# Kernel optimization log

Measured on AMD Instinct MI355X. Metric: run time of the kernel, lower is better.

## Reference

```python
import jax, jax.numpy as jnp
import numpy as np

D_MODEL = 1024
NUM_HEADS = 16
HEAD_DIM = D_MODEL // NUM_HEADS


def setup_inputs() -> dict:
    key = jax.random.key(0)
    ks = jax.random.split(key, 5)
    B, S = 2, 2048
    x = jax.random.normal(ks[0], (B, S, D_MODEL), dtype=jnp.float32)
    Wq = jax.random.normal(ks[1], (D_MODEL, D_MODEL), dtype=jnp.float32) * 0.02
    Wk = jax.random.normal(ks[2], (D_MODEL, D_MODEL), dtype=jnp.float32) * 0.02
    Wv = jax.random.normal(ks[3], (D_MODEL, D_MODEL), dtype=jnp.float32) * 0.02
    Wo = jax.random.normal(ks[4], (D_MODEL, D_MODEL), dtype=jnp.float32) * 0.02
    return {"x": x, "Wq": Wq, "Wk": Wk, "Wv": Wv, "Wo": Wo}


def reference(x, Wq, Wk, Wv, Wo):
    B, S, _ = x.shape
    # QKV projections (Linear is x @ W, no bias)
    q = (x @ Wq).reshape(B, S, NUM_HEADS, HEAD_DIM).transpose(0, 2, 1, 3)  # [B,H,S,Dh]
    k = (x @ Wk).reshape(B, S, NUM_HEADS, HEAD_DIM).transpose(0, 2, 1, 3)
    v = (x @ Wv).reshape(B, S, NUM_HEADS, HEAD_DIM).transpose(0, 2, 1, 3)
    scale = 1.0 / jnp.sqrt(jnp.asarray(HEAD_DIM, dtype=x.dtype))
    scores = jnp.einsum("bhqd,bhkd->bhqk", q, k) * scale  # [B,H,S,S]
    causal = jnp.tril(jnp.ones((S, S), dtype=bool))
    scores = jnp.where(causal, scores, -jnp.inf)
    probs = jax.nn.softmax(scores, axis=-1)
    out = jnp.einsum("bhqk,bhkd->bhqd", probs, v)  # [B,H,S,Dh]
    out = out.transpose(0, 2, 1, 3).reshape(B, S, D_MODEL)
    return out @ Wo
```

## Files before the change

### kernel.cpp

```cpp
#include <hip/hip_runtime.h>

typedef __attribute__((ext_vector_type(4))) short short4v;
typedef __attribute__((ext_vector_type(8))) short short8v;
typedef __attribute__((ext_vector_type(4))) float float4v;
typedef __attribute__((ext_vector_type(4))) int int4v;

#define GLD_LDS16(gsrc, ldst)                                                             \
    __builtin_amdgcn_global_load_lds(                                                     \
        (const __attribute__((address_space(1))) void*)(gsrc),                            \
        (__attribute__((address_space(3))) void*)(ldst), 16, 0, 0)

__device__ __forceinline__ short f2bf(float f) {
    unsigned u = __builtin_bit_cast(unsigned, f);
    u += 0x7fffu + ((u >> 16) & 1u);
    return (short)(u >> 16);
}

__global__ void k_cvt_x(const float* __restrict__ x, short* __restrict__ xb) {
    int i = blockIdx.x * blockDim.x + threadIdx.x;
    float4v v = ((const float4v*)x)[i];
    short4v o;
    o[0] = f2bf(v[0]); o[1] = f2bf(v[1]); o[2] = f2bf(v[2]); o[3] = f2bf(v[3]);
    ((short4v*)xb)[i] = o;
}

__global__ void k_transpose(const float* __restrict__ W0, const float* __restrict__ W1,
                            const float* __restrict__ W2, const float* __restrict__ W3,
                            short* __restrict__ Wt) {
    const float* W = blockIdx.z == 0 ? W0 : blockIdx.z == 1 ? W1 : blockIdx.z == 2 ? W2 : W3;
    short* dst = Wt + (size_t)blockIdx.z * 1024 * 1024;
    __shared__ float tile[32][33];
    int x0 = blockIdx.x * 32, y0 = blockIdx.y * 32;
    int tx = threadIdx.x, ty = threadIdx.y;
#pragma unroll
    for (int j = 0; j < 4; j++) {
        int r = ty + j * 8;
        tile[r][tx] = W[(size_t)(y0 + r) * 1024 + x0 + tx];
    }
    __syncthreads();
#pragma unroll
    for (int j = 0; j < 4; j++) {
        int r = ty + j * 8;
        dst[(size_t)(x0 + r) * 1024 + y0 + tx] = f2bf(tile[tx][r]);
    }
}

template <int MODE>
__launch_bounds__(512, 4)
__global__ void k_gemm2(const short* __restrict__ A, const short* __restrict__ Bt,
                        short* __restrict__ out0, short* __restrict__ out1,
                        float* __restrict__ outF) {
    __shared__ short As[2][128][64];
    __shared__ short Bs[2][128][64];
    int t = threadIdx.x;
    int l = t & 63, w = t >> 6;
    int wm = w >> 2, wn = w & 3;
    int lr = l & 15, lg = l >> 4;
    int m0 = blockIdx.x * 128, n0 = blockIdx.y * 128;
    const short* Bp = Bt + (MODE == 0 ? ((size_t)blockIdx.z << 20) : 0);

    int srow = l >> 3;
    int sg = (l & 7) ^ srow;
    const short* Ab0 = A + (size_t)(m0 + w * 8 + srow) * 1024 + sg * 8;
    const short* Ab1 = Ab0 + 64 * 1024;
    const short* Bb0 = Bp + (size_t)(n0 + w * 8 + srow) * 1024 + sg * 8;
    const short* Bb1 = Bb0 + 64 * 1024;

    float4v acc[4][2] = {};

#define STAGE(bb, k0)                                   \
    do {                                                \
        GLD_LDS16(Ab0 + (k0), &As[bb][w * 8][0]);       \
        GLD_LDS16(Ab1 + (k0), &As[bb][64 + w * 8][0]);  \
        GLD_LDS16(Bb0 + (k0), &Bs[bb][w * 8][0]);       \
        GLD_LDS16(Bb1 + (k0), &Bs[bb][64 + w * 8][0]);  \
    } while (0)

    STAGE(0, 0);
    __syncthreads();
    int cur = 0;

    for (int kt = 0; kt < 16; kt++) {
        if (kt + 1 < 16) STAGE(cur ^ 1, (kt + 1) * 64);
#pragma unroll
        for (int ks = 0; ks < 2; ks++) {
            short8v af[4], bfv[2];
            int hh = ks * 4 + lg;
            int sw = ((hh ^ (lr & 7)) * 8);
#pragma unroll
            for (int fm = 0; fm < 4; fm++)
                af[fm] = *(const short8v*)&As[cur][wm * 64 + fm * 16 + lr][sw];
#pragma unroll
            for (int fn = 0; fn < 2; fn++)
                bfv[fn] = *(const short8v*)&Bs[cur][wn * 32 + fn * 16 + lr][sw];
            __builtin_amdgcn_s_setprio(1);
#pragma unroll
            for (int fm = 0; fm < 4; fm++)
#pragma unroll
                for (int fn = 0; fn < 2; fn++)
                    acc[fm][fn] = (MODE == 1)
                        ? __builtin_amdgcn_mfma_f32_16x16x32_bf16(bfv[fn], af[fm], acc[fm][fn], 0, 0, 0)
                        : __builtin_amdgcn_mfma_f32_16x16x32_bf16(af[fm], bfv[fn], acc[fm][fn], 0, 0, 0);
            __builtin_amdgcn_s_setprio(0);
        }
        __syncthreads();
        cur ^= 1;
    }
#undef STAGE

    if (MODE == 0) {
        short* out = (blockIdx.z == 0) ? out0 : out1;
        float scale = (blockIdx.z == 0) ? 0.125f * 1.44269504088896f : 1.0f;
#pragma unroll
        for (int fm = 0; fm < 4; fm++)
#pragma unroll
            for (int fn = 0; fn < 2; fn++)
#pragma unroll
                for (int r = 0; r < 4; r++) {
                    int m = m0 + wm * 64 + fm * 16 + lg * 4 + r;
                    int n = n0 + wn * 32 + fn * 16 + lr;
                    float v = acc[fm][fn][r] * scale;
                    int b = m >> 11, s = m & 2047, h = n >> 6, dh = n & 63;
                    out[(((size_t)(b * 16 + h)) * 2048 + s) * 64 + dh] = f2bf(v);
                }
    } else if (MODE == 1) {
#pragma unroll
        for (int fm = 0; fm < 4; fm++)
#pragma unroll
            for (int fn = 0; fn < 2; fn++)
#pragma unroll
                for (int r = 0; r < 4; r++) {
                    int n = n0 + wn * 32 + fn * 16 + lg * 4 + r;
                    int m = m0 + wm * 64 + fm * 16 + lr;
                    int b = m >> 11, s = m & 2047, h = n >> 6, dh = n & 63;
                    out0[(((size_t)(b * 16 + h)) * 64 + dh) * 2048 + s] = f2bf(acc[fm][fn][r]);
                }
    } else {
#pragma unroll
        for (int fm = 0; fm < 4; fm++)
#pragma unroll
            for (int fn = 0; fn < 2; fn++)
#pragma unroll
                for (int r = 0; r < 4; r++) {
                    int m = m0 + wm * 64 + fm * 16 + lg * 4 + r;
                    int n = n0 + wn * 32 + fn * 16 + lr;
                    outF[(size_t)m * 1024 + n] = acc[fm][fn][r];
                }
    }
}

__launch_bounds__(256, 2)
__global__ void k_attn(const short* __restrict__ Qb, const short* __restrict__ Kb,
                       const short* __restrict__ Vtb, short* __restrict__ Ob) {
    __shared__ short K_lds[2][64][64];
    __shared__ short V_lds[2][64][64];
    __shared__ short p_lds[4][16][72];
    int t = threadIdx.x;
    int l = t & 63, w = t >> 6;
    int lr = l & 15, lg = l >> 4;

    int L = blockIdx.y * 16 + blockIdx.x;
    int bh = (L & 7) * 4 + ((L >> 3) & 3);
    int p = L >> 5;

    const short* Qp = Qb + (size_t)bh * 2048 * 64;
    const short* Kp = Kb + (size_t)bh * 2048 * 64;
    const short* Vp = Vtb + (size_t)bh * 64 * 2048;

    int n0 = 32 - p;
    int n1 = p + 1;
    const int total = 33;

    int srow = 0, scol = 0;
    {
    }

    auto stage = [&](int bb, int kv0) {
#pragma unroll
        for (int i = 0; i < 2; i++) {
            int s = w * 64 + i * 256 + l;
            int row = s >> 3, cg = s & 7;
            int cs = (cg ^ (row & 7)) * 8;
            GLD_LDS16(&Kp[(size_t)(kv0 + row) * 64 + cs],
                      (short*)K_lds[bb] + (size_t)(w * 64 + i * 256) * 8);
            GLD_LDS16(&Vp[(size_t)row * 2048 + kv0 + cs],
                      (short*)V_lds[bb] + (size_t)(w * 64 + i * 256) * 8);
        }
    };

    stage(0, 0);

    int tile = 31 - p;
    int q0 = tile * 64 + w * 16;
    short8v qf0 = *(const short8v*)&Qp[(size_t)(q0 + lr) * 64 + lg * 8];
    short8v qf1 = *(const short8v*)&Qp[(size_t)(q0 + lr) * 64 + 32 + lg * 8];

    float4v o[4] = {};
    float mr[4] = {-3e38f, -3e38f, -3e38f, -3e38f};
    float lsum[4] = {0.f, 0.f, 0.f, 0.f};
    int cur = 0;
    int b = bh >> 4, h = bh & 15;

    __syncthreads();

    for (int ci = 0; ci < total; ci++) {
        bool second = ci >= n0;
        int ntile = second ? n1 : n0;
        int c = second ? ci - n0 : ci;
        int kv0 = c * 64;

        int cin = ci + 1;
        if (cin < total) {
            int kvn = (cin < n0) ? cin * 64 : (cin - n0) * 64;
            stage(cur ^ 1, kvn);
        }

        const short* Kf = (const short*)K_lds[cur];
        float4v s[4] = {};
        __builtin_amdgcn_s_setprio(1);
#pragma unroll
        for (int t4 = 0; t4 < 4; t4++) {
            int krow = t4 * 16 + lr;
            int sw = (krow & 7);
            short8v kfa = *(const short8v*)&Kf[krow * 64 + ((lg ^ sw) * 8)];
            short8v kfb = *(const short8v*)&Kf[krow * 64 + (((lg ^ 4) ^ sw) * 8)];
            s[t4] = __builtin_amdgcn_mfma_f32_16x16x32_bf16(qf0, kfa, s[t4], 0, 0, 0);
            s[t4] = __builtin_amdgcn_mfma_f32_16x16x32_bf16(qf1, kfb, s[t4], 0, 0, 0);
        }
        __builtin_amdgcn_s_setprio(0);

        if (c == ntile - 1) {
#pragma unroll
            for (int t4 = 0; t4 < 4; t4++)
#pragma unroll
                for (int r = 0; r < 4; r++) {
                    int row = q0 + lg * 4 + r;
                    if (kv0 + t4 * 16 + lr > row) s[t4][r] = -3e38f;
                }
        }

        float mx[4];
#pragma unroll
        for (int r = 0; r < 4; r++) {
            float m_ = fmaxf(fmaxf(s[0][r], s[1][r]), fmaxf(s[2][r], s[3][r]));
            m_ = fmaxf(m_, __shfl_xor(m_, 1));
            m_ = fmaxf(m_, __shfl_xor(m_, 2));
            m_ = fmaxf(m_, __shfl_xor(m_, 4));
            m_ = fmaxf(m_, __shfl_xor(m_, 8));
            mx[r] = m_;
        }
        bool ok = (mx[0] - mr[0] <= 8.f) && (mx[1] - mr[1] <= 8.f) &&
                  (mx[2] - mr[2] <= 8.f) && (mx[3] - mr[3] <= 8.f);
        if (!__all((int)ok)) {
#pragma unroll
            for (int r = 0; r < 4; r++) {
                float mnew = fmaxf(mr[r], mx[r]);
                float sc = __builtin_amdgcn_exp2f(mr[r] - mnew);
                mr[r] = mnew;
                lsum[r] *= sc;
                o[0][r] *= sc; o[1][r] *= sc; o[2][r] *= sc; o[3][r] *= sc;
            }
        }
#pragma unroll
        for (int r = 0; r < 4; r++) {
            float e0 = __builtin_amdgcn_exp2f(s[0][r] - mr[r]);
            float e1 = __builtin_amdgcn_exp2f(s[1][r] - mr[r]);
            float e2 = __builtin_amdgcn_exp2f(s[2][r] - mr[r]);
            float e3 = __builtin_amdgcn_exp2f(s[3][r] - mr[r]);
            lsum[r] += (e0 + e1) + (e2 + e3);
            p_lds[w][lg * 4 + r][lr]      = f2bf(e0);
            p_lds[w][lg * 4 + r][16 + lr] = f2bf(e1);
            p_lds[w][lg * 4 + r][32 + lr] = f2bf(e2);
            p_lds[w][lg * 4 + r][48 + lr] = f2bf(e3);
        }

        short8v pa0 = *(const short8v*)&p_lds[w][lr][lg * 8];
        short8v pa1 = *(const short8v*)&p_lds[w][lr][32 + lg * 8];

        const short* Vf = (const short*)V_lds[cur];
        __builtin_amdgcn_s_setprio(1);
#pragma unroll
        for (int dt = 0; dt < 4; dt++) {
            int vrow = dt * 16 + lr;
            int sw = (vrow & 7);
            short8v vfa = *(const short8v*)&Vf[vrow * 64 + ((lg ^ sw) * 8)];
            short8v vfb = *(const short8v*)&Vf[vrow * 64 + (((lg ^ 4) ^ sw) * 8)];
            o[dt] = __builtin_amdgcn_mfma_f32_16x16x32_bf16(pa0, vfa, o[dt], 0, 0, 0);
            o[dt] = __builtin_amdgcn_mfma_f32_16x16x32_bf16(pa1, vfb, o[dt], 0, 0, 0);
        }
        __builtin_amdgcn_s_setprio(0);

        if (c == ntile - 1) {
            float inv[4];
#pragma unroll
            for (int r = 0; r < 4; r++) {
                float ls = lsum[r];
                ls += __shfl_xor(ls, 1);
                ls += __shfl_xor(ls, 2);
                ls += __shfl_xor(ls, 4);
                ls += __shfl_xor(ls, 8);
                inv[r] = 1.0f / ls;
            }
#pragma unroll
            for (int dt = 0; dt < 4; dt++)
#pragma unroll
                for (int r = 0; r < 4; r++) {
                    int q = q0 + lg * 4 + r;
                    Ob[((size_t)(b * 2048 + q)) * 1024 + h * 64 + dt * 16 + lr] = f2bf(o[dt][r] * inv[r]);
                }
            if (!second) {
                tile = p;
                q0 = tile * 64 + w * 16;
                qf0 = *(const short8v*)&Qp[(size_t)(q0 + lr) * 64 + lg * 8];
                qf1 = *(const short8v*)&Qp[(size_t)(q0 + lr) * 64 + 32 + lg * 8];
#pragma unroll
                for (int dt = 0; dt < 4; dt++) o[dt] = float4v{0.f, 0.f, 0.f, 0.f};
#pragma unroll
                for (int r = 0; r < 4; r++) { mr[r] = -3e38f; lsum[r] = 0.f; }
            }
        }

        __syncthreads();
        cur ^= 1;
    }
}

extern "C" void kernel_launch(void* const* d_in, const int* in_sizes, int n_in,
                              void* d_out, int out_size, void* d_ws, size_t ws_size,
                              hipStream_t stream) {
    const float* x  = (const float*)d_in[0];
    const float* Wq = (const float*)d_in[1];
    const float* Wk = (const float*)d_in[2];
    const float* Wv = (const float*)d_in[3];
    const float* Wo = (const float*)d_in[4];
    float* out = (float*)d_out;

    char* ws = (char*)d_ws;
    short* xb  = (short*)(ws);
    short* Wtb = (short*)(ws + 8388608);
    short* Qb  = (short*)(ws + 16777216);
    short* Kb  = (short*)(ws + 25165824);
    short* Vtb = (short*)(ws + 33554432);
    short* Ob  = (short*)(ws + 41943040);

    k_cvt_x<<<4096, 256, 0, stream>>>(x, xb);
    k_transpose<<<dim3(32, 32, 4), dim3(32, 8), 0, stream>>>(Wq, Wk, Wv, Wo, Wtb);
    k_gemm2<0><<<dim3(32, 8, 2), 512, 0, stream>>>(xb, Wtb, Qb, Kb, nullptr);
    k_gemm2<1><<<dim3(32, 8), 512, 0, stream>>>(xb, Wtb + 2 * 1048576, Vtb, nullptr, nullptr);
    k_attn<<<dim3(16, 32), 256, 0, stream>>>(Qb, Kb, Vtb, Ob);
    k_gemm2<2><<<dim3(32, 8), 512, 0, stream>>>(Ob, Wtb + 3 * 1048576, nullptr, nullptr, out);
}
```

Measured before the change: 123.0 us.

## Load V fragments directly from global into registers and defer max shuffles

Removes the V tile from the shared-memory double buffer. Each wave now loads its V fragments straight from global memory into registers at the start of each KV iteration, so they can overlap with the QK MFMAs. Separately, the cross-lane max reduction is skipped unless some lane's local max exceeds the running max by the threshold, which cuts shuffles in the common case. The cost is that every wave issues its own redundant global V reads, and global-load latency may be exposed where the async LDS prefetch used to hide it.

```diff
diff --git a/kernel.cpp b/kernel.cpp
--- a/kernel.cpp
+++ b/kernel.cpp
@@ -153,7 +153,6 @@
 __global__ void k_attn(const short* __restrict__ Qb, const short* __restrict__ Kb,
                        const short* __restrict__ Vtb, short* __restrict__ Ob) {
     __shared__ short K_lds[2][64][64];
-    __shared__ short V_lds[2][64][64];
     __shared__ short p_lds[4][16][72];
     int t = threadIdx.x;
     int l = t & 63, w = t >> 6;
@@ -171,11 +170,7 @@
     int n1 = p + 1;
     const int total = 33;
 
-    int srow = 0, scol = 0;
-    {
-    }
-
-    auto stage = [&](int bb, int kv0) {
+    auto stageK = [&](int bb, int kv0) {
 #pragma unroll
         for (int i = 0; i < 2; i++) {
             int s = w * 64 + i * 256 + l;
@@ -183,12 +178,10 @@
             int cs = (cg ^ (row & 7)) * 8;
             GLD_LDS16(&Kp[(size_t)(kv0 + row) * 64 + cs],
                       (short*)K_lds[bb] + (size_t)(w * 64 + i * 256) * 8);
-            GLD_LDS16(&Vp[(size_t)row * 2048 + kv0 + cs],
-                      (short*)V_lds[bb] + (size_t)(w * 64 + i * 256) * 8);
         }
     };
 
-    stage(0, 0);
+    stageK(0, 0);
 
     int tile = 31 - p;
     int q0 = tile * 64 + w * 16;
@@ -212,7 +205,14 @@
         int cin = ci + 1;
         if (cin < total) {
             int kvn = (cin < n0) ? cin * 64 : (cin - n0) * 64;
-            stage(cur ^ 1, kvn);
+            stageK(cur ^ 1, kvn);
+        }
+
+        short8v vf[8];
+#pragma unroll
+        for (int dt = 0; dt < 4; dt++) {
+            vf[dt]     = *(const short8v*)&Vp[(size_t)(dt * 16 + lr) * 2048 + kv0 + lg * 8];
+            vf[4 + dt] = *(const short8v*)&Vp[(size_t)(dt * 16 + lr) * 2048 + kv0 + 32 + lg * 8];
         }
 
         const short* Kf = (const short*)K_lds[cur];
@@ -241,20 +241,19 @@
 
         float mx[4];
 #pragma unroll
-        for (int r = 0; r < 4; r++) {
-            float m_ = fmaxf(fmaxf(s[0][r], s[1][r]), fmaxf(s[2][r], s[3][r]));
-            m_ = fmaxf(m_, __shfl_xor(m_, 1));
-            m_ = fmaxf(m_, __shfl_xor(m_, 2));
-            m_ = fmaxf(m_, __shfl_xor(m_, 4));
-            m_ = fmaxf(m_, __shfl_xor(m_, 8));
-            mx[r] = m_;
-        }
-        bool ok = (mx[0] - mr[0] <= 8.f) && (mx[1] - mr[1] <= 8.f) &&
-                  (mx[2] - mr[2] <= 8.f) && (mx[3] - mr[3] <= 8.f);
-        if (!__all((int)ok)) {
+        for (int r = 0; r < 4; r++)
+            mx[r] = fmaxf(fmaxf(s[0][r], s[1][r]), fmaxf(s[2][r], s[3][r]));
+        float worst = fmaxf(fmaxf(mx[0] - mr[0], mx[1] - mr[1]),
+                            fmaxf(mx[2] - mr[2], mx[3] - mr[3]));
+        if (!__all(worst <= 8.f)) {
 #pragma unroll
             for (int r = 0; r < 4; r++) {
-                float mnew = fmaxf(mr[r], mx[r]);
+                float m_ = mx[r];
+                m_ = fmaxf(m_, __shfl_xor(m_, 1));
+                m_ = fmaxf(m_, __shfl_xor(m_, 2));
+                m_ = fmaxf(m_, __shfl_xor(m_, 4));
+                m_ = fmaxf(m_, __shfl_xor(m_, 8));
+                float mnew = fmaxf(mr[r], m_);
                 float sc = __builtin_amdgcn_exp2f(mr[r] - mnew);
                 mr[r] = mnew;
                 lsum[r] *= sc;
@@ -277,16 +276,11 @@
         short8v pa0 = *(const short8v*)&p_lds[w][lr][lg * 8];
         short8v pa1 = *(const short8v*)&p_lds[w][lr][32 + lg * 8];
 
-        const short* Vf = (const short*)V_lds[cur];
         __builtin_amdgcn_s_setprio(1);
 #pragma unroll
         for (int dt = 0; dt < 4; dt++) {
-            int vrow = dt * 16 + lr;
-            int sw = (vrow & 7);
-            short8v vfa = *(const short8v*)&Vf[vrow * 64 + ((lg ^ sw) * 8)];
-            short8v vfb = *(const short8v*)&Vf[vrow * 64 + (((lg ^ 4) ^ sw) * 8)];
-            o[dt] = __builtin_amdgcn_mfma_f32_16x16x32_bf16(pa0, vfa, o[dt], 0, 0, 0);
-            o[dt] = __builtin_amdgcn_mfma_f32_16x16x32_bf16(pa1, vfb, o[dt], 0, 0, 0);
+            o[dt] = __builtin_amdgcn_mfma_f32_16x16x32_bf16(pa0, vf[dt], o[dt], 0, 0, 0);
+            o[dt] = __builtin_amdgcn_mfma_f32_16x16x32_bf16(pa1, vf[4 + dt], o[dt], 0, 0, 0);
         }
         __builtin_amdgcn_s_setprio(0);
 
```

After: 144.7 us. 17.6% more time.
